# Kernel optimization log

Hardware: AMD Instinct MI355X
Metric: run time of the kernel (lower is better)

Reference implementation:

```python
import jax, jax.numpy as jnp
import numpy as np

N_NODES = 50000
N_EDGES = 250000
D_OBJ = 128   # input_dim_obj
D_PRED = 128  # input_dim_pred
D_OUT = 128   # output_dim
K_STEPS = 2   # k_update_steps


def setup_inputs() -> dict:
    key = jax.random.key(0)
    ks = jax.random.split(key, 12)
    obj_vecs = jax.random.normal(ks[0], (N_NODES, D_OBJ), jnp.float32)
    pred_vecs = jax.random.normal(ks[1], (N_EDGES, D_PRED), jnp.float32)
    src = jax.random.randint(ks[2], (N_EDGES,), 0, N_NODES)
    # ensure every node has in-degree >= 1 (matches DGL reduce firing on all nodes)
    dst = jnp.concatenate([jnp.arange(N_NODES),
                           jax.random.randint(ks[3], (N_EDGES - N_NODES,), 0, N_NODES)])
    edges = jnp.stack([src, dst], axis=1).astype(jnp.int64)

    def w(k, fi, fo):
        return jax.random.normal(k, (fi, fo), jnp.float32) / np.sqrt(fi).astype(np.float32)

    return {
        "obj_vecs": obj_vecs,
        "pred_vecs": pred_vecs,
        "edges": edges,
        "W_node": w(ks[4], D_OBJ, D_OBJ),        # linear_node
        "W_obj_score": w(ks[5], D_OBJ, 1),       # object_score
        "W_edge": w(ks[6], D_PRED, D_OBJ),       # linear_edge
        "W_rel_score": w(ks[7], D_OBJ, 1),       # relation_score
        "W_phi_node": w(ks[8], 2 * D_OBJ, D_OBJ),  # linear_phi_node
        "W_phi_edge": w(ks[9], 2 * D_OBJ, D_PRED), # linear_phi_edge
        "W_node_out": w(ks[10], D_OBJ, D_OUT),   # node_out_net
        "W_edge_out": w(ks[11], D_PRED, D_OUT),  # edge_out_net
    }


def _gat_forward(obj_vecs, pred_vecs, src, dst,
                 W_node, W_obj_score, W_edge, W_rel_score,
                 W_phi_node, W_phi_edge, W_node_out, W_edge_out):
    F_n = obj_vecs           # [N, D_OBJ]
    F_e_t = pred_vecs        # [E, D_PRED]
    for _ in range(K_STEPS):
        F_n = F_n @ W_node                       # linear_node
        F_e_new = F_e_t @ W_edge                 # linear_edge -> [E, D_OBJ]
        s_n = F_n @ W_obj_score                  # [N, 1]
        s_e = F_e_new @ W_rel_score              # [E, 1]

        F_src = F_n[src]                         # [E, D_OBJ]
        F_dst = F_n[dst]
        s_src = s_n[src]                         # [E, 1]
        s_dst = s_n[dst]

        # --- edge update (io_attention_send, update_relations branch) ---
        # softmax over the (src, dst) pair per edge
        a = jax.nn.softmax(jnp.stack([s_src, s_dst], axis=1), axis=1)   # [E, 2, 1]
        applied_e = jnp.sum(a * jnp.stack([F_src, F_dst], axis=1), axis=1)  # [E, D_OBJ]
        F_e_next = jax.nn.relu(jnp.concatenate([applied_e, F_e_new], axis=-1) @ W_phi_edge)

        # --- node update (io_attention_reduce): segment softmax over
        # BOTH the per-edge src-node scores and edge scores, grouped by dst ---
        m = jax.ops.segment_max(jnp.maximum(s_src, s_e)[:, 0], dst,
                                num_segments=N_NODES)                  # [N]
        m = jax.lax.stop_gradient(m)[dst][:, None]                     # [E, 1]
        e_n = jnp.exp(s_src - m)                                       # [E, 1]
        e_e = jnp.exp(s_e - m)
        num = jax.ops.segment_sum(e_n * F_src + e_e * F_e_new, dst,
                                  num_segments=N_NODES)                # [N, D_OBJ]
        den = jax.ops.segment_sum((e_n + e_e)[:, 0], dst,
                                  num_segments=N_NODES)[:, None]       # [N, 1]
        applied_n = num / den
        F_n = jax.nn.relu(jnp.concatenate([applied_n, F_n], axis=-1) @ W_phi_node)
        F_e_t = F_e_next

    return F_n @ W_node_out, F_e_t @ W_edge_out


def reference(obj_vecs, pred_vecs, edges,
              W_node, W_obj_score, W_edge, W_rel_score,
              W_phi_node, W_phi_edge, W_node_out, W_edge_out):
    src = edges[:, 0]
    dst = edges[:, 1]
    return _gat_forward(obj_vecs, pred_vecs, src, dst,
                        W_node, W_obj_score, W_edge, W_rel_score,
                        W_phi_node, W_phi_edge, W_node_out, W_edge_out)
```

## Files before the change

### kernel.cpp

```cpp
#include <hip/hip_runtime.h>

#define NN 50000
#define NE 250000

typedef __bf16 bf16_8 __attribute__((ext_vector_type(8)));
typedef __bf16 bf16_2 __attribute__((ext_vector_type(2)));
typedef float  f32x4  __attribute__((ext_vector_type(4)));

__device__ __forceinline__ int swz(int row, int bc) {
    return row * 256 + (bc ^ ((row & 7) << 4));
}

__global__ __launch_bounds__(256) void wprep(const float* __restrict__ W,
                                             __bf16* __restrict__ Wt, int K) {
    int idx = blockIdx.x * 256 + threadIdx.x;
    if (idx >= 128 * K) return;
    int c = idx / K, k = idx % K;
    Wt[idx] = (__bf16)W[(size_t)k * 128 + c];
}

__global__ __launch_bounds__(256) void csr_count(const int* __restrict__ edges,
                                                 unsigned* __restrict__ counts) {
    int e = blockIdx.x * 256 + threadIdx.x;
    if (e < NE) atomicAdd(&counts[edges[2 * e + 1]], 1u);
}

__global__ __launch_bounds__(256) void csr_scan(const unsigned* __restrict__ counts,
                                                unsigned* __restrict__ offs) {
    __shared__ unsigned partial[257];
    const int t = threadIdx.x;
    const int chunk = (NN + 255) / 256;
    const int lo = t * chunk;
    const int hi = (lo + chunk < NN) ? lo + chunk : NN;
    unsigned s = 0;
    for (int i = lo; i < hi; ++i) s += counts[i];
    partial[t + 1] = s;
    if (t == 0) partial[0] = 0;
    __syncthreads();
    if (t == 0)
        for (int i = 1; i <= 256; ++i) partial[i] += partial[i - 1];
    __syncthreads();
    unsigned run = partial[t];
    for (int i = lo; i < hi; ++i) { offs[i] = run; run += counts[i]; }
    if (t == 255) offs[NN] = run;
}

__global__ __launch_bounds__(256) void csr_fill(const int* __restrict__ edges,
                                                unsigned* __restrict__ cursor,
                                                int* __restrict__ csr) {
    int e = blockIdx.x * 256 + threadIdx.x;
    if (e >= NE) return;
    int d = edges[2 * e + 1];
    unsigned p = atomicAdd(&cursor[d], 1u);
    csr[p] = e;
}

template<int KH, bool A0F32, bool RELU, bool SCORE, bool OUTF32>
__global__ __launch_bounds__(256, 2) void mfma_gemm(
    const void* __restrict__ A0, const void* __restrict__ A1,
    const __bf16* __restrict__ Wt, const float* __restrict__ wsc,
    void* __restrict__ out, float* __restrict__ sout, int M)
{
    __shared__ __align__(16) char smem[65536];
    __shared__ float sred[128];
    char* As = smem;
    char* Ws = smem + 32768;

    const int t = threadIdx.x;
    const int rowbase = blockIdx.x * 128;
    const int wv = t >> 6, lane = t & 63;
    const int wr = (wv >> 1) * 64, wc = (wv & 1) * 64;
    const int lr = lane & 15, kq = lane >> 4;

    if (SCORE && t < 128) sred[t] = 0.0f;

    f32x4 acc[4][4] = {};

#pragma unroll
    for (int h = 0; h < KH; ++h) {
        if (h) __syncthreads();
        const char* Asrc = (h == 0) ? (const char*)A0 : (const char*)A1;
        const bool srcF32 = (h == 0) && A0F32;
#pragma unroll
        for (int i = 0; i < 8; ++i) {
            int flat = (i * 256 + t) * 8;
            int row = flat >> 7, k = flat & 127;
            int grow = rowbase + row; if (grow > M - 1) grow = M - 1;
            bf16_8 v;
            if (srcF32) {
                const float* p = (const float*)Asrc + (size_t)grow * 128 + k;
                float4 u0 = *(const float4*)p, u1 = *(const float4*)(p + 4);
                v[0] = (__bf16)u0.x; v[1] = (__bf16)u0.y;
                v[2] = (__bf16)u0.z; v[3] = (__bf16)u0.w;
                v[4] = (__bf16)u1.x; v[5] = (__bf16)u1.y;
                v[6] = (__bf16)u1.z; v[7] = (__bf16)u1.w;
            } else {
                v = *(const bf16_8*)((const __bf16*)Asrc + (size_t)grow * 128 + k);
            }
            *(bf16_8*)(As + swz(row, k * 2)) = v;
        }
#pragma unroll
        for (int i = 0; i < 8; ++i) {
            int flat = (i * 256 + t) * 8;
            int c = flat >> 7, k = flat & 127;
            bf16_8 v = *(const bf16_8*)(Wt + (size_t)c * (KH * 128) + h * 128 + k);
            *(bf16_8*)(Ws + swz(c, k * 2)) = v;
        }
        __syncthreads();
#pragma unroll
        for (int ks = 0; ks < 4; ++ks) {
            const int bc = ks * 64 + kq * 16;
            bf16_8 a[4], b[4];
#pragma unroll
            for (int ra = 0; ra < 4; ++ra)
                a[ra] = *(const bf16_8*)(As + swz(wr + 16 * ra + lr, bc));
#pragma unroll
            for (int cb = 0; cb < 4; ++cb)
                b[cb] = *(const bf16_8*)(Ws + swz(wc + 16 * cb + lr, bc));
#pragma unroll
            for (int ra = 0; ra < 4; ++ra)
#pragma unroll
                for (int cb = 0; cb < 4; ++cb)
                    acc[ra][cb] = __builtin_amdgcn_mfma_f32_16x16x32_bf16(
                        a[ra], b[cb], acc[ra][cb], 0, 0, 0);
        }
    }

#pragma unroll
    for (int ra = 0; ra < 4; ++ra)
#pragma unroll
        for (int cb = 0; cb < 4; ++cb) {
            const int col = wc + 16 * cb + lr;
#pragma unroll
            for (int r = 0; r < 4; ++r) {
                const int row = rowbase + wr + 16 * ra + kq * 4 + r;
                float v = acc[ra][cb][r];
                if (RELU) v = fmaxf(v, 0.0f);
                if (row < M) {
                    if (OUTF32) ((float*)out)[(size_t)row * 128 + col] = v;
                    else ((__bf16*)out)[(size_t)row * 128 + col] = (__bf16)v;
                }
            }
        }
    if (SCORE) {
        float wsv[4];
#pragma unroll
        for (int cb = 0; cb < 4; ++cb) wsv[cb] = wsc[wc + 16 * cb + lr];
#pragma unroll
        for (int ra = 0; ra < 4; ++ra)
#pragma unroll
            for (int r = 0; r < 4; ++r) {
                float part = acc[ra][0][r] * wsv[0] + acc[ra][1][r] * wsv[1]
                           + acc[ra][2][r] * wsv[2] + acc[ra][3][r] * wsv[3];
                part += __shfl_xor(part, 1); part += __shfl_xor(part, 2);
                part += __shfl_xor(part, 4); part += __shfl_xor(part, 8);
                if (lr == 0)
                    atomicAdd(&sred[wr + 16 * ra + kq * 4 + r], part);
            }
        __syncthreads();
        if (t < 128 && rowbase + t < M) sout[rowbase + t] = sred[t];
    }
}

__global__ __launch_bounds__(256) void edge_apply_kernel(
    const __bf16* __restrict__ Fn, const float* __restrict__ sn,
    const int* __restrict__ edges, __bf16* __restrict__ applied)
{
    const int t = threadIdx.x;
    const int sub = t & 15;
    const int e = blockIdx.x * 16 + (t >> 4);
    if (e >= NE) return;
    const int src = edges[2 * e];
    const int dst = edges[2 * e + 1];
    const float ss = sn[src], sd = sn[dst];
    const float mx = fmaxf(ss, sd);
    const float p0 = expf(ss - mx), p1 = expf(sd - mx);
    const float inv = 1.0f / (p0 + p1);
    const float a0 = p0 * inv, a1 = p1 * inv;
    bf16_8 fs = *(const bf16_8*)(Fn + (size_t)src * 128 + sub * 8);
    bf16_8 fd = *(const bf16_8*)(Fn + (size_t)dst * 128 + sub * 8);
    bf16_8 o;
#pragma unroll
    for (int j = 0; j < 8; ++j)
        o[j] = (__bf16)(a0 * (float)fs[j] + a1 * (float)fd[j]);
    *(bf16_8*)(applied + (size_t)e * 128 + sub * 8) = o;
}

__global__ __launch_bounds__(256) void aggregate_kernel(
    const int* __restrict__ edges, const int* __restrict__ csr,
    const unsigned* __restrict__ offs, const __bf16* __restrict__ FnN,
    const float* __restrict__ s_n, const float* __restrict__ s_e,
    const __bf16* __restrict__ FeN, __bf16* __restrict__ applied_n)
{
    const int t = threadIdx.x;
    const int lane = t & 63;
    const int n = blockIdx.x * 4 + (t >> 6);
    if (n >= NN) return;
    const unsigned beg = offs[n], end = offs[n + 1];

    float m = -1e30f;
    for (unsigned i = beg + lane; i < end; i += 64) {
        int e = csr[i];
        int src = edges[2 * e];
        m = fmaxf(m, fmaxf(s_n[src], s_e[e]));
    }
#pragma unroll
    for (int msk = 32; msk >= 1; msk >>= 1) m = fmaxf(m, __shfl_xor(m, msk));

    float a0 = 0.f, a1 = 0.f, dn = 0.f;
    for (unsigned i = beg; i < end; ++i) {
        int e = csr[i];
        int src = edges[2 * e];
        float en = expf(s_n[src] - m), ee = expf(s_e[e] - m);
        bf16_2 fs = *(const bf16_2*)(FnN + (size_t)src * 128 + lane * 2);
        bf16_2 fe = *(const bf16_2*)(FeN + (size_t)e * 128 + lane * 2);
        a0 += en * (float)fs[0] + ee * (float)fe[0];
        a1 += en * (float)fs[1] + ee * (float)fe[1];
        dn += en + ee;
    }
    const float inv = 1.0f / dn;
    bf16_2 o;
    o[0] = (__bf16)(a0 * inv);
    o[1] = (__bf16)(a1 * inv);
    *(bf16_2*)(applied_n + (size_t)n * 128 + lane * 2) = o;
}

extern "C" void kernel_launch(void* const* d_in, const int* in_sizes, int n_in,
                              void* d_out, int out_size, void* d_ws, size_t ws_size,
                              hipStream_t stream)
{
    const float* obj         = (const float*)d_in[0];
    const float* pred        = (const float*)d_in[1];
    const int*   edges       = (const int*)d_in[2];
    const float* W_node      = (const float*)d_in[3];
    const float* W_obj_score = (const float*)d_in[4];
    const float* W_edge      = (const float*)d_in[5];
    const float* W_rel_score = (const float*)d_in[6];
    const float* W_phi_node  = (const float*)d_in[7];
    const float* W_phi_edge  = (const float*)d_in[8];
    const float* W_node_out  = (const float*)d_in[9];
    const float* W_edge_out  = (const float*)d_in[10];
    float* out = (float*)d_out;

    char*  ws  = (char*)d_ws;
    size_t off = 0;
    auto alloc = [&](size_t nbytes) -> void* {
        void* p = ws + off;
        off = (off + nbytes + 255) & ~(size_t)255;
        return p;
    };
    __bf16*   FnA   = (__bf16*)alloc((size_t)NN * 128 * 2);
    __bf16*   FnN   = (__bf16*)alloc((size_t)NN * 128 * 2);
    __bf16*   FnApp = (__bf16*)alloc((size_t)NN * 128 * 2);
    float*    s_n   = (float*)alloc((size_t)NN * 4);
    __bf16*   FeA   = (__bf16*)alloc((size_t)NE * 128 * 2);
    __bf16*   FeN   = (__bf16*)alloc((size_t)NE * 128 * 2);
    float*    s_e   = (float*)alloc((size_t)NE * 4);
    unsigned* counts = (unsigned*)alloc((size_t)NN * 4);
    unsigned* offs   = (unsigned*)alloc((size_t)(NN + 1) * 4);
    unsigned* cursor = (unsigned*)alloc((size_t)NN * 4);
    int*      csr    = (int*)alloc((size_t)NE * 4);
    __bf16*   Wn_t  = (__bf16*)alloc((size_t)128 * 128 * 2);
    __bf16*   We_t  = (__bf16*)alloc((size_t)128 * 128 * 2);
    __bf16*   Wpn_t = (__bf16*)alloc((size_t)128 * 256 * 2);
    __bf16*   Wpe_t = (__bf16*)alloc((size_t)128 * 256 * 2);
    __bf16*   Wno_t = (__bf16*)alloc((size_t)128 * 128 * 2);
    __bf16*   Weo_t = (__bf16*)alloc((size_t)128 * 128 * 2);
    (void)ws_size; (void)in_sizes; (void)n_in; (void)out_size;

    wprep<<<64, 256, 0, stream>>>(W_node, Wn_t, 128);
    wprep<<<64, 256, 0, stream>>>(W_edge, We_t, 128);
    wprep<<<128, 256, 0, stream>>>(W_phi_node, Wpn_t, 256);
    wprep<<<128, 256, 0, stream>>>(W_phi_edge, Wpe_t, 256);
    wprep<<<64, 256, 0, stream>>>(W_node_out, Wno_t, 128);
    wprep<<<64, 256, 0, stream>>>(W_edge_out, Weo_t, 128);

    const int eB = (NE + 255) / 256;
    hipMemsetAsync(counts, 0, (size_t)NN * 4, stream);
    csr_count<<<eB, 256, 0, stream>>>(edges, counts);
    csr_scan<<<1, 256, 0, stream>>>(counts, offs);
    hipMemcpyAsync(cursor, offs, (size_t)NN * 4, hipMemcpyDeviceToDevice, stream);
    csr_fill<<<eB, 256, 0, stream>>>(edges, cursor, csr);

    const int nodeBlocks = (NN + 127) / 128;
    const int edgeBlocks = (NE + 127) / 128;
    const int eBlocks16  = (NE + 15) / 16;
    const int aggBlocks  = (NN + 3) / 4;

    for (int step = 0; step < 2; ++step) {
        if (step == 0)
            mfma_gemm<1, true, false, true, false><<<nodeBlocks, 256, 0, stream>>>(
                obj, nullptr, Wn_t, W_obj_score, FnN, s_n, NN);
        else
            mfma_gemm<1, false, false, true, false><<<nodeBlocks, 256, 0, stream>>>(
                FnA, nullptr, Wn_t, W_obj_score, FnN, s_n, NN);
        if (step == 0)
            mfma_gemm<1, true, false, true, false><<<edgeBlocks, 256, 0, stream>>>(
                pred, nullptr, We_t, W_rel_score, FeN, s_e, NE);
        else
            mfma_gemm<1, false, false, true, false><<<edgeBlocks, 256, 0, stream>>>(
                FeA, nullptr, We_t, W_rel_score, FeN, s_e, NE);
        edge_apply_kernel<<<eBlocks16, 256, 0, stream>>>(FnN, s_n, edges, FeA);
        aggregate_kernel<<<aggBlocks, 256, 0, stream>>>(
            edges, csr, offs, FnN, s_n, s_e, FeN, FnApp);
        mfma_gemm<2, false, true, false, false><<<edgeBlocks, 256, 0, stream>>>(
            FeA, FeN, Wpe_t, nullptr, FeA, nullptr, NE);
        mfma_gemm<2, false, true, false, false><<<nodeBlocks, 256, 0, stream>>>(
            FnApp, FnN, Wpn_t, nullptr, FnA, nullptr, NN);
    }

    mfma_gemm<1, false, false, false, true><<<nodeBlocks, 256, 0, stream>>>(
        FnA, nullptr, Wno_t, nullptr, out, nullptr, NN);
    mfma_gemm<1, false, false, false, true><<<edgeBlocks, 256, 0, stream>>>(
        FeA, nullptr, Weo_t, nullptr, out + (size_t)NN * 128, nullptr, NE);
}
```

Baseline: 762.4 us.

## Merge paired GEMMs into dual launches and fuse edge-apply into phi-edge GEMM

```diff
diff --git a/kernel.cpp b/kernel.cpp
--- a/kernel.cpp
+++ b/kernel.cpp
@@ -55,19 +55,36 @@
     csr[p] = e;
 }
 
-template<int KH, bool A0F32, bool RELU, bool SCORE, bool OUTF32>
-__global__ __launch_bounds__(256, 2) void mfma_gemm(
-    const void* __restrict__ A0, const void* __restrict__ A1,
-    const __bf16* __restrict__ Wt, const float* __restrict__ wsc,
-    void* __restrict__ out, float* __restrict__ sout, int M)
+template<int KH, bool A0F32, bool APPLY, bool RELU, bool SCORE, bool OUTF32>
+__global__ __launch_bounds__(256, 2) void mfma_gemm_dual(
+    const void* __restrict__ A0a, const void* __restrict__ A1a,
+    const __bf16* __restrict__ Wta, const float* __restrict__ wsca,
+    void* __restrict__ outa, float* __restrict__ souta, int Ma,
+    int blocksA, int applyA,
+    const void* __restrict__ A0b, const void* __restrict__ A1b,
+    const __bf16* __restrict__ Wtb, const float* __restrict__ wscb,
+    void* __restrict__ outb, float* __restrict__ soutb, int Mb, int applyB,
+    const int* __restrict__ edges, const float* __restrict__ sn,
+    const __bf16* __restrict__ FnN)
 {
     __shared__ __align__(16) char smem[65536];
     __shared__ float sred[128];
     char* As = smem;
     char* Ws = smem + 32768;
 
+    const int b = blockIdx.x;
+    const bool isA = (b < blocksA);
+    const void* A0 = isA ? A0a : A0b;
+    const void* A1 = isA ? A1a : A1b;
+    const __bf16* Wt = isA ? Wta : Wtb;
+    const float* wsc = isA ? wsca : wscb;
+    void* out  = isA ? outa : outb;
+    float* sout = isA ? souta : soutb;
+    const int M = isA ? Ma : Mb;
+    const int apply = isA ? applyA : applyB;
+    const int rowbase = (isA ? b : b - blocksA) * 128;
+
     const int t = threadIdx.x;
-    const int rowbase = blockIdx.x * 128;
     const int wv = t >> 6, lane = t & 63;
     const int wr = (wv >> 1) * 64, wc = (wv & 1) * 64;
     const int lr = lane & 15, kq = lane >> 4;
@@ -81,13 +98,26 @@
         if (h) __syncthreads();
         const char* Asrc = (h == 0) ? (const char*)A0 : (const char*)A1;
         const bool srcF32 = (h == 0) && A0F32;
+        const bool doApply = APPLY && (h == 0) && (apply != 0);
 #pragma unroll
         for (int i = 0; i < 8; ++i) {
             int flat = (i * 256 + t) * 8;
             int row = flat >> 7, k = flat & 127;
             int grow = rowbase + row; if (grow > M - 1) grow = M - 1;
             bf16_8 v;
-            if (srcF32) {
+            if (APPLY && doApply) {
+                int src = edges[2 * grow], dst = edges[2 * grow + 1];
+                float ss = sn[src], sd = sn[dst];
+                float mx = fmaxf(ss, sd);
+                float p0 = expf(ss - mx), p1 = expf(sd - mx);
+                float inv = 1.0f / (p0 + p1);
+                float a0 = p0 * inv, a1 = p1 * inv;
+                bf16_8 fs = *(const bf16_8*)(FnN + (size_t)src * 128 + k);
+                bf16_8 fd = *(const bf16_8*)(FnN + (size_t)dst * 128 + k);
+#pragma unroll
+                for (int j = 0; j < 8; ++j)
+                    v[j] = (__bf16)(a0 * (float)fs[j] + a1 * (float)fd[j]);
+            } else if (srcF32) {
                 const float* p = (const float*)Asrc + (size_t)grow * 128 + k;
                 float4 u0 = *(const float4*)p, u1 = *(const float4*)(p + 4);
                 v[0] = (__bf16)u0.x; v[1] = (__bf16)u0.y;
@@ -110,19 +140,19 @@
 #pragma unroll
         for (int ks = 0; ks < 4; ++ks) {
             const int bc = ks * 64 + kq * 16;
-            bf16_8 a[4], b[4];
+            bf16_8 a[4], bb[4];
 #pragma unroll
             for (int ra = 0; ra < 4; ++ra)
                 a[ra] = *(const bf16_8*)(As + swz(wr + 16 * ra + lr, bc));
 #pragma unroll
             for (int cb = 0; cb < 4; ++cb)
-                b[cb] = *(const bf16_8*)(Ws + swz(wc + 16 * cb + lr, bc));
+                bb[cb] = *(const bf16_8*)(Ws + swz(wc + 16 * cb + lr, bc));
 #pragma unroll
             for (int ra = 0; ra < 4; ++ra)
 #pragma unroll
                 for (int cb = 0; cb < 4; ++cb)
                     acc[ra][cb] = __builtin_amdgcn_mfma_f32_16x16x32_bf16(
-                        a[ra], b[cb], acc[ra][cb], 0, 0, 0);
+                        a[ra], bb[cb], acc[ra][cb], 0, 0, 0);
         }
     }
 
@@ -160,30 +190,6 @@
         __syncthreads();
         if (t < 128 && rowbase + t < M) sout[rowbase + t] = sred[t];
     }
-}
-
-__global__ __launch_bounds__(256) void edge_apply_kernel(
-    const __bf16* __restrict__ Fn, const float* __restrict__ sn,
-    const int* __restrict__ edges, __bf16* __restrict__ applied)
-{
-    const int t = threadIdx.x;
-    const int sub = t & 15;
-    const int e = blockIdx.x * 16 + (t >> 4);
-    if (e >= NE) return;
-    const int src = edges[2 * e];
-    const int dst = edges[2 * e + 1];
-    const float ss = sn[src], sd = sn[dst];
-    const float mx = fmaxf(ss, sd);
-    const float p0 = expf(ss - mx), p1 = expf(sd - mx);
-    const float inv = 1.0f / (p0 + p1);
-    const float a0 = p0 * inv, a1 = p1 * inv;
-    bf16_8 fs = *(const bf16_8*)(Fn + (size_t)src * 128 + sub * 8);
-    bf16_8 fd = *(const bf16_8*)(Fn + (size_t)dst * 128 + sub * 8);
-    bf16_8 o;
-#pragma unroll
-    for (int j = 0; j < 8; ++j)
-        o[j] = (__bf16)(a0 * (float)fs[j] + a1 * (float)fd[j]);
-    *(bf16_8*)(applied + (size_t)e * 128 + sub * 8) = o;
 }
 
 __global__ __launch_bounds__(256) void aggregate_kernel(
@@ -284,33 +290,30 @@
 
     const int nodeBlocks = (NN + 127) / 128;
     const int edgeBlocks = (NE + 127) / 128;
-    const int eBlocks16  = (NE + 15) / 16;
+    const int dualBlocks = nodeBlocks + edgeBlocks;
     const int aggBlocks  = (NN + 3) / 4;
 
     for (int step = 0; step < 2; ++step) {
         if (step == 0)
-            mfma_gemm<1, true, false, true, false><<<nodeBlocks, 256, 0, stream>>>(
-                obj, nullptr, Wn_t, W_obj_score, FnN, s_n, NN);
+            mfma_gemm_dual<1, true, false, false, true, false><<<dualBlocks, 256, 0, stream>>>(
+                obj,  nullptr, Wn_t, W_obj_score, FnN, s_n, NN, nodeBlocks, 0,
+                pred, nullptr, We_t, W_rel_score, FeN, s_e, NE, 0,
+                nullptr, nullptr, nullptr);
         else
-            mfma_gemm<1, false, false, true, false><<<nodeBlocks, 256, 0, stream>>>(
-                FnA, nullptr, Wn_t, W_obj_score, FnN, s_n, NN);
-        if (step == 0)
-            mfma_gemm<1, true, false, true, false><<<edgeBlocks, 256, 0, stream>>>(
-                pred, nullptr, We_t, W_rel_score, FeN, s_e, NE);
-        else
-            mfma_gemm<1, false, false, true, false><<<edgeBlocks, 256, 0, stream>>>(
-                FeA, nullptr, We_t, W_rel_score, FeN, s_e, NE);
-        edge_apply_kernel<<<eBlocks16, 256, 0, stream>>>(FnN, s_n, edges, FeA);
+            mfma_gemm_dual<1, false, false, false, true, false><<<dualBlocks, 256, 0, stream>>>(
+                FnA, nullptr, Wn_t, W_obj_score, FnN, s_n, NN, nodeBlocks, 0,
+                FeA, nullptr, We_t, W_rel_score, FeN, s_e, NE, 0,
+                nullptr, nullptr, nullptr);
         aggregate_kernel<<<aggBlocks, 256, 0, stream>>>(
             edges, csr, offs, FnN, s_n, s_e, FeN, FnApp);
-        mfma_gemm<2, false, true, false, false><<<edgeBlocks, 256, 0, stream>>>(
-            FeA, FeN, Wpe_t, nullptr, FeA, nullptr, NE);
-        mfma_gemm<2, false, true, false, false><<<nodeBlocks, 256, 0, stream>>>(
-            FnApp, FnN, Wpn_t, nullptr, FnA, nullptr, NN);
-    }
-
-    mfma_gemm<1, false, false, false, true><<<nodeBlocks, 256, 0, stream>>>(
-        FnA, nullptr, Wno_t, nullptr, out, nullptr, NN);
-    mfma_gemm<1, false, false, false, true><<<edgeBlocks, 256, 0, stream>>>(
-        FeA, nullptr, Weo_t, nullptr, out + (size_t)NN * 128, nullptr, NE);
-}
+        mfma_gemm_dual<2, false, true, true, false, false><<<dualBlocks, 256, 0, stream>>>(
+            nullptr, FeN, Wpe_t, nullptr, FeA, nullptr, NE, edgeBlocks, 1,
+            FnApp,   FnN, Wpn_t, nullptr, FnA, nullptr, NN, 0,
+            edges, s_n, FnN);
+    }
+
+    mfma_gemm_dual<1, false, false, false, false, true><<<dualBlocks, 256, 0, stream>>>(
+        FnA, nullptr, Wno_t, nullptr, out, nullptr, NN, nodeBlocks, 0,
+        FeA, nullptr, Weo_t, nullptr, out + (size_t)NN * 128, nullptr, NE, 0,
+        nullptr, nullptr, nullptr);
+}
```

Result: faster. 725.4 us (-4.9%).
